# Kernel optimization log

Measured on AMD Instinct MI355X. Metric: run time of the kernel, lower is better.

Reference implementation:

```python
import jax, jax.numpy as jnp
import numpy as np

EPS = 1e-5

def _bn(x, g, b):
    # training-mode BatchNorm3d over (N, T, H, W) per channel (axis=1), biased variance
    red = (0, 2, 3, 4)
    m = x.mean(red, keepdims=True)
    v = x.var(red, keepdims=True)
    s = (1, -1, 1, 1, 1)
    return (x - m) / jnp.sqrt(v + EPS) * g.reshape(s) + b.reshape(s)

def _conv3d(x, w, b):
    # Conv3d kernel (1,3,3), padding (0,1,1)
    y = jax.lax.conv_general_dilated(x, w, (1, 1, 1), ((0, 0), (1, 1), (1, 1)),
                                     dimension_numbers=('NCDHW', 'OIDHW', 'NCDHW'))
    return y + b[None, :, None, None, None]

def _forward(x1, x2, attn_weight, W_up, b_up, W_mlp, b_mlp, g_mlp, be_mlp,
             W_c1, b_c1, g_c1, be_c1, W_c2, b_c2, g_c2, be_c2):
    w2 = W_up[:, :, 0]  # [Cin, Cout, 2, 2]
    y = jnp.einsum('bcthw,cokl->bothkwl', x1, w2)
    b_, o, t, h, k, w_, l = y.shape
    x1u = y.reshape(b_, o, t, h * k, w_ * l) + b_up[None, :, None, None, None]

    bs, d_in, T, H, W = x2.shape
    nH = attn_weight.shape[0]
    hh, ww = attn_weight.shape[2], attn_weight.shape[3]
    # [nH, bs, h, w, T, T] -> [nH*bs, T*T, h, w], bilinear upsample to (H, W)
    A = attn_weight.transpose(0, 1, 4, 5, 2, 3).reshape(nH * bs, T * T, hh, ww)
    A = jax.image.resize(A, (nH * bs, T * T, H, W), method='linear')
    A = A.reshape(nH, bs, T, T, H, W)
    # per-(head,b,H,W) temporal attention matmul: avoids materializing x2.repeat(n_head,...)
    ctx = jnp.einsum('nbtsxy,bcsxy->btxycn', A, x2)  # [bs,T,H,W,d_in,nH]
    ctx = ctx.reshape(bs, T, H, W, d_in * nH)        # flatten order (c, n) matches torch permute+view
    hmlp = jnp.einsum('btxyk,ko->btxyo', ctx, W_mlp) + b_mlp
    hmlp = hmlp.transpose(0, 4, 1, 2, 3)  # [bs, enc, T, H, W]
    hmlp = jax.nn.relu(_bn(hmlp, g_mlp, be_mlp))

    x = jnp.concatenate([hmlp, x1u], axis=1)  # [bs, enc+dec, T, H, W]
    x = jax.nn.relu(_bn(_conv3d(x, W_c1, b_c1), g_c1, be_c1))
    x = jax.nn.relu(_bn(_conv3d(x, W_c2, b_c2), g_c2, be_c2))
    return x

def setup_inputs() -> dict:
    key = jax.random.key(0)
    ks = jax.random.split(key, 8)
    bs, T, H, W = 2, 8, 128, 128
    dec, enc, nH = 64, 32, 4
    hh = ww = 16  # attn_scale_factor = 8
    return {
        'x1': jax.random.normal(ks[0], (bs, dec, T, H // 2, W // 2), jnp.float32),
        'x2': jax.random.normal(ks[1], (bs, enc, T, H, W), jnp.float32),
        'attn_weight': jax.random.uniform(ks[2], (nH, bs, hh, ww, T, T), jnp.float32),
        'W_up': jax.random.normal(ks[3], (dec, dec, 1, 2, 2), jnp.float32) * 0.05,
        'b_up': jnp.zeros((dec,), jnp.float32),
        'W_mlp': jax.random.normal(ks[4], (nH * enc, enc), jnp.float32) * 0.05,
        'b_mlp': jnp.zeros((enc,), jnp.float32),
        'g_mlp': jnp.ones((enc,), jnp.float32),
        'be_mlp': jnp.zeros((enc,), jnp.float32),
        'W_c1': jax.random.normal(ks[5], (enc, dec + enc, 1, 3, 3), jnp.float32) * 0.05,
        'b_c1': jnp.zeros((enc,), jnp.float32),
        'g_c1': jnp.ones((enc,), jnp.float32),
        'be_c1': jnp.zeros((enc,), jnp.float32),
        'W_c2': jax.random.normal(ks[6], (enc, enc, 1, 3, 3), jnp.float32) * 0.05,
        'b_c2': jnp.zeros((enc,), jnp.float32),
        'g_c2': jnp.ones((enc,), jnp.float32),
        'be_c2': jnp.zeros((enc,), jnp.float32),
    }

def reference(x1, x2, attn_weight, W_up, b_up, W_mlp, b_mlp, g_mlp, be_mlp,
              W_c1, b_c1, g_c1, be_c1, W_c2, b_c2, g_c2, be_c2):
    return _forward(x1, x2, attn_weight, W_up, b_up, W_mlp, b_mlp, g_mlp, be_mlp,
                    W_c1, b_c1, g_c1, be_c1, W_c2, b_c2, g_c2, be_c2)
```

## Files before the change

kernel.cpp:

```cpp
#include <hip/hip_runtime.h>


#define EPSV 1e-5f

typedef __attribute__((ext_vector_type(8))) short short8;
typedef __attribute__((ext_vector_type(4))) float floatx4;

__device__ inline short f2bf(float f) {
  union { float f; unsigned u; } v; v.f = f;
  unsigned r = (v.u + 0x7fffu + ((v.u >> 16) & 1u)) >> 16;
  return (short)r;
}
__device__ inline float bf2f(short s) {
  union { unsigned u; float f; } v; v.u = ((unsigned)(unsigned short)s) << 16;
  return v.f;
}

#define U_OFF    0
#define HMB_OFF  16777216
#define C1B_OFF  20971520
#define WB1_OFF  25165824
#define WB2_OFF  25179648
#define ST_OFF   25184256
#define SC_OFF   25184448

__global__ __launch_bounds__(256) void k_up(const float* __restrict__ x1,
        const float* __restrict__ Wup, const float* __restrict__ bup,
        float* __restrict__ U) {
  int bid = blockIdx.x;
  int hw = (bid & 15) * 256 + threadIdx.x;
  int t = (bid >> 4) & 7;
  int o = (bid >> 7) & 63;
  int b = bid >> 13;
  int h = hw >> 6, w = hw & 63;
  const float4* W4 = (const float4*)Wup;
  const float* xp = x1 + (b*64*8 + t)*4096 + hw;
  float a00=0.f, a01=0.f, a10=0.f, a11=0.f;
  #pragma unroll 8
  for (int c=0;c<64;++c) {
    float xv = xp[c*32768];
    float4 wv = W4[c*64+o];
    a00 = fmaf(xv, wv.x, a00);
    a01 = fmaf(xv, wv.y, a01);
    a10 = fmaf(xv, wv.z, a10);
    a11 = fmaf(xv, wv.w, a11);
  }
  float bb = bup[o];
  float* up = U + ((b*64+o)*8+t)*16384 + h*256 + w*2;
  ((float2*)up)[0]       = make_float2(a00+bb, a01+bb);
  ((float2*)(up+128))[0] = make_float2(a10+bb, a11+bb);
}

__global__ __launch_bounds__(256) void k_ctxmlp(const float* __restrict__ x2,
        const float* __restrict__ attn, const float* __restrict__ Wmlp,
        const float* __restrict__ bmlp, short* __restrict__ HMb) {
  int t = blockIdx.y, b = blockIdx.z;
  int pos = blockIdx.x*256 + threadIdx.x;
  __shared__ float la[8192];
  float4* la4 = (float4*)la;
  const float4* g4 = (const float4*)attn;
  #pragma unroll
  for (int k=0;k<8;++k) {
    int i = k*256 + (int)threadIdx.x;
    int s4 = i & 1, iy = (i>>1)&15, ix = (i>>5)&15, n = i>>9;
    la4[i] = g4[((((n*2+b)*16+ix)*16+iy)*8+t)*2 + s4];
  }
  __syncthreads();
  int x = pos >> 7, y = pos & 127;
  float ux = (x+0.5f)*0.125f - 0.5f;
  float uy = (y+0.5f)*0.125f - 0.5f;
  int ix0 = (int)floorf(ux), iy0 = (int)floorf(uy);
  float fx = ux - (float)ix0, fy = uy - (float)iy0;
  int ixa = max(ix0,0), ixb = min(ix0+1,15);
  int iya = max(iy0,0), iyb = min(iy0+1,15);
  float w00=(1.f-fx)*(1.f-fy), w01=(1.f-fx)*fy, w10=fx*(1.f-fy), w11=fx*fy;
  float a[4][8];
  #pragma unroll
  for (int n=0;n<4;++n) {
    const float4* p00 = la4 + ((n*16+ixa)*16+iya)*2;
    const float4* p01 = la4 + ((n*16+ixa)*16+iyb)*2;
    const float4* p10 = la4 + ((n*16+ixb)*16+iya)*2;
    const float4* p11 = la4 + ((n*16+ixb)*16+iyb)*2;
    #pragma unroll
    for (int q=0;q<2;++q) {
      float4 c00=p00[q], c01=p01[q], c10=p10[q], c11=p11[q];
      a[n][q*4+0] = w00*c00.x + w01*c01.x + w10*c10.x + w11*c11.x;
      a[n][q*4+1] = w00*c00.y + w01*c01.y + w10*c10.y + w11*c11.y;
      a[n][q*4+2] = w00*c00.z + w01*c01.z + w10*c10.z + w11*c11.z;
      a[n][q*4+3] = w00*c00.w + w01*c01.w + w10*c10.w + w11*c11.w;
    }
  }
  float acc[32];
  #pragma unroll
  for (int o=0;o<32;++o) acc[o] = bmlp[o];
  const float* x2p = x2 + b*4194304 + pos;
  #pragma unroll 4
  for (int c=0;c<32;++c) {
    float xr[8];
    #pragma unroll
    for (int s=0;s<8;++s) xr[s] = x2p[(c*8+s)*16384];
    #pragma unroll
    for (int n=0;n<4;++n) {
      float ctx = 0.f;
      #pragma unroll
      for (int s=0;s<8;++s) ctx = fmaf(a[n][s], xr[s], ctx);
      const float* wrow = Wmlp + (c*4+n)*32;
      #pragma unroll
      for (int o=0;o<32;++o) acc[o] = fmaf(ctx, wrow[o], acc[o]);
    }
  }
  short8* hp = (short8*)(HMb + ((long)((b*8+t)*16384 + pos)) * 32);
  #pragma unroll
  for (int g=0; g<4; ++g) {
    short8 v;
    #pragma unroll
    for (int j=0;j<8;++j) v[j] = f2bf(acc[g*8+j]);
    hp[g] = v;
  }
}

__global__ __launch_bounds__(256) void k_stats_cl(const unsigned* __restrict__ src, float* __restrict__ st) {
  __shared__ float sb[64];
  if (threadIdx.x < 64) sb[threadIdx.x] = 0.f;
  __syncthreads();
  int cp = threadIdx.x & 15;
  int pg = threadIdx.x >> 4;
  long pbase = (long)blockIdx.x * 256;
  float s0=0.f,q0=0.f,s1=0.f,q1=0.f;
  #pragma unroll 4
  for (int it = 0; it < 16; ++it) {
    long pos = pbase + it*16 + pg;
    unsigned d = src[pos*16 + cp];
    float v0 = bf2f((short)(d & 0xffffu));
    float v1 = bf2f((short)(d >> 16));
    s0+=v0; q0+=v0*v0; s1+=v1; q1+=v1*v1;
  }
  s0 += __shfl_xor(s0,16); s0 += __shfl_xor(s0,32);
  q0 += __shfl_xor(q0,16); q0 += __shfl_xor(q0,32);
  s1 += __shfl_xor(s1,16); s1 += __shfl_xor(s1,32);
  q1 += __shfl_xor(q1,16); q1 += __shfl_xor(q1,32);
  if ((threadIdx.x & 63) < 16) {
    atomicAdd(&sb[2*cp],    s0); atomicAdd(&sb[2*cp+1],    s1);
    atomicAdd(&sb[32+2*cp], q0); atomicAdd(&sb[32+2*cp+1], q1);
  }
  __syncthreads();
  if (threadIdx.x < 64) atomicAdd(&st[threadIdx.x], sb[threadIdx.x]);
}

__global__ __launch_bounds__(256) void k_stats(const float* __restrict__ src, float* __restrict__ st) {
  int bid = blockIdx.x;
  int span = bid & 31, ch = (bid>>5)&31, b = bid>>10;
  const float4* p4 = (const float4*)(src + (b*32+ch)*131072 + span*4096);
  float s=0.f, q=0.f;
  #pragma unroll
  for (int k=0;k<4;++k) {
    float4 v = p4[k*256 + threadIdx.x];
    s += v.x+v.y+v.z+v.w;
    q += v.x*v.x + v.y*v.y + v.z*v.z + v.w*v.w;
  }
  #pragma unroll
  for (int off=32; off>0; off>>=1) { s += __shfl_down(s,off); q += __shfl_down(q,off); }
  __shared__ float ls[4], lq[4];
  int lane = threadIdx.x & 63, wv = threadIdx.x >> 6;
  if (lane==0) { ls[wv]=s; lq[wv]=q; }
  __syncthreads();
  if (threadIdx.x==0) {
    atomicAdd(&st[ch],    ls[0]+ls[1]+ls[2]+ls[3]);
    atomicAdd(&st[32+ch], lq[0]+lq[1]+lq[2]+lq[3]);
  }
}

__global__ void k_finalize(const float* __restrict__ st, const float* __restrict__ g,
                           const float* __restrict__ be, float* __restrict__ sc, float* __restrict__ sh) {
  int c = threadIdx.x;
  if (c < 32) {
    float mean = st[c] * (1.f/262144.f);
    float var  = st[32+c] * (1.f/262144.f) - mean*mean;
    float s = g[c] / sqrtf(var + EPSV);
    sc[c] = s;
    sh[c] = be[c] - mean*s;
  }
}

__global__ __launch_bounds__(256) void k_repackb(const float* __restrict__ Wc1, const float* __restrict__ Wc2,
        short* __restrict__ wb1, short* __restrict__ wb2) {
  int i = blockIdx.x*256 + threadIdx.x;
  if (i < 27648) {
    int cc = i / 9216, r = i % 9216;
    int tap = r / 1024, r2 = r % 1024;
    int nt = r2 >> 9, lane = (r2 >> 3) & 63, j = r2 & 7;
    int o = nt*16 + (lane & 15);
    int cin = cc*32 + (lane >> 4)*8 + j;
    wb1[i] = f2bf(Wc1[(o*96 + cin)*9 + tap]);
  }
  if (i < 9216) {
    int tap = i / 1024, r2 = i % 1024;
    int nt = r2 >> 9, lane = (r2 >> 3) & 63, j = r2 & 7;
    int o = nt*16 + (lane & 15);
    int cin = (lane >> 4)*8 + j;
    wb2[i] = f2bf(Wc2[(o*32 + cin)*9 + tap]);
  }
}

template<int NCHUNK, bool FIRST>
__global__ __launch_bounds__(256) void k_conv_mfma(
    const short* __restrict__ srcCL, const float* __restrict__ srcU,
    const short* __restrict__ wb, const float* __restrict__ bias,
    const float* __restrict__ sc, const float* __restrict__ sh,
    short* __restrict__ dstCL, float* __restrict__ dstP) {
  constexpr int SMEM = FIRST ? 25920 : 33792;
  __shared__ __align__(16) char smem[SMEM];
  short* stage = (short*)smem;

  int t = blockIdx.y, b = blockIdx.z;
  int x0 = (int)(blockIdx.x >> 3) * 16, y0 = (int)(blockIdx.x & 7) * 16;
  int tid = threadIdx.x, lane = tid & 63, w = tid >> 6;

  float bias0 = bias[lane & 15], bias1 = bias[16 + (lane & 15)];
  floatx4 acc[4][2];
  #pragma unroll
  for (int mt=0; mt<4; ++mt) {
    acc[mt][0] = (floatx4){bias0,bias0,bias0,bias0};
    acc[mt][1] = (floatx4){bias1,bias1,bias1,bias1};
  }

  for (int cc=0; cc<NCHUNK; ++cc) {
    __syncthreads();
    if (cc == 0) {
      #pragma unroll
      for (int g=0; g<4; ++g) {
        float s0=sc[g*8+0],s1=sc[g*8+1],s2=sc[g*8+2],s3=sc[g*8+3];
        float s4=sc[g*8+4],s5=sc[g*8+5],s6=sc[g*8+6],s7=sc[g*8+7];
        float h0=sh[g*8+0],h1=sh[g*8+1],h2=sh[g*8+2],h3=sh[g*8+3];
        float h4=sh[g*8+4],h5=sh[g*8+5],h6=sh[g*8+6],h7=sh[g*8+7];
        for (int p=tid; p<324; p+=256) {
          int r = p/18, c = p - r*18;
          int X = x0 - 1 + r, Y = y0 - 1 + c;
          short8 val = (short8)0;
          if ((unsigned)X < 128u && (unsigned)Y < 128u) {
            short8 raw = *(const short8*)(srcCL + (((long)(b*8+t)*16384 + X*128 + Y) * 32 + g*8));
            val[0]=f2bf(fmaxf(fmaf(bf2f(raw[0]),s0,h0),0.f));
            val[1]=f2bf(fmaxf(fmaf(bf2f(raw[1]),s1,h1),0.f));
            val[2]=f2bf(fmaxf(fmaf(bf2f(raw[2]),s2,h2),0.f));
            val[3]=f2bf(fmaxf(fmaf(bf2f(raw[3]),s3,h3),0.f));
            val[4]=f2bf(fmaxf(fmaf(bf2f(raw[4]),s4,h4),0.f));
            val[5]=f2bf(fmaxf(fmaf(bf2f(raw[5]),s5,h5),0.f));
            val[6]=f2bf(fmaxf(fmaf(bf2f(raw[6]),s6,h6),0.f));
            val[7]=f2bf(fmaxf(fmaf(bf2f(raw[7]),s7,h7),0.f));
          }
          *(short8*)(stage + p*40 + g*8) = val;
        }
      }
    } else {
      int cbase = (cc-1)*32;
      #pragma unroll
      for (int g=0; g<4; ++g) {
        for (int p=tid; p<324; p+=256) {
          int r = p/18, c = p - r*18;
          int X = x0 - 1 + r, Y = y0 - 1 + c;
          short8 val = (short8)0;
          if ((unsigned)X < 128u && (unsigned)Y < 128u) {
            const float* up = srcU + ((long)(b*64 + cbase + g*8)*8 + t)*16384 + X*128 + Y;
            #pragma unroll
            for (int j=0;j<8;++j) val[j] = f2bf(up[(long)j*131072]);
          }
          *(short8*)(stage + p*40 + g*8) = val;
        }
      }
    }
    __syncthreads();
    const short8* wbp = (const short8*)wb + (long)cc*9*2*64;
    #pragma unroll
    for (int tap=0; tap<9; ++tap) {
      int dy = tap/3, dx = tap - dy*3;
      short8 b0 = wbp[(tap*2+0)*64 + lane];
      short8 b1 = wbp[(tap*2+1)*64 + lane];
      #pragma unroll
      for (int mt=0; mt<4; ++mt) {
        int p = (w*4 + mt + dy)*18 + (lane & 15) + dx;
        short8 a = *(const short8*)(stage + p*40 + (lane>>4)*8);
        acc[mt][0] = __builtin_amdgcn_mfma_f32_16x16x32_bf16(a, b0, acc[mt][0], 0,0,0);
        acc[mt][1] = __builtin_amdgcn_mfma_f32_16x16x32_bf16(a, b1, acc[mt][1], 0,0,0);
      }
    }
  }

  __syncthreads();
  if (FIRST) {
    short* tr = (short*)smem;
    #pragma unroll
    for (int mt=0; mt<4; ++mt) {
      int prow = w*4 + mt;
      #pragma unroll
      for (int nt=0; nt<2; ++nt) {
        #pragma unroll
        for (int r=0; r<4; ++r) {
          int m = (lane>>4)*4 + r;
          tr[(prow*16 + m)*32 + nt*16 + (lane&15)] = f2bf(acc[mt][nt][r]);
        }
      }
    }
    __syncthreads();
    int px = tid >> 4, py = tid & 15;
    short8* d8 = (short8*)(dstCL + (((long)(b*8+t)*128 + x0+px)*128 + (y0+py))*32);
    const short8* s8 = (const short8*)(tr + tid*32);
    d8[0]=s8[0]; d8[1]=s8[1]; d8[2]=s8[2]; d8[3]=s8[3];
  } else {
    float* trf = (float*)smem;
    #pragma unroll
    for (int mt=0; mt<4; ++mt) {
      int prow = w*4 + mt;
      #pragma unroll
      for (int nt=0; nt<2; ++nt) {
        #pragma unroll
        for (int r=0; r<4; ++r) {
          int m = (lane>>4)*4 + r;
          trf[(prow*16 + m)*33 + nt*16 + (lane&15)] = acc[mt][nt][r];
        }
      }
    }
    __syncthreads();
    int px = tid >> 4, py = tid & 15;
    #pragma unroll
    for (int ch=0; ch<32; ++ch) {
      dstP[((long)(b*32+ch)*8 + t)*16384 + (x0+px)*128 + (y0+py)] = trf[tid*33 + ch];
    }
  }
}

__global__ __launch_bounds__(256) void k_bnrelu(float* __restrict__ out,
        const float* __restrict__ sc, const float* __restrict__ sh) {
  int i = blockIdx.x*256 + threadIdx.x;
  int ch = (i >> 15) & 31;
  float s = sc[ch], h = sh[ch];
  float4* p = (float4*)out;
  float4 v = p[i];
  v.x = fmaxf(fmaf(v.x,s,h),0.f);
  v.y = fmaxf(fmaf(v.y,s,h),0.f);
  v.z = fmaxf(fmaf(v.z,s,h),0.f);
  v.w = fmaxf(fmaf(v.w,s,h),0.f);
  p[i] = v;
}

extern "C" void kernel_launch(void* const* d_in, const int* in_sizes, int n_in,
                              void* d_out, int out_size, void* d_ws, size_t ws_size,
                              hipStream_t stream) {
  (void)in_sizes; (void)n_in; (void)out_size; (void)ws_size;
  const float* x1   = (const float*)d_in[0];
  const float* x2   = (const float*)d_in[1];
  const float* attn = (const float*)d_in[2];
  const float* Wup  = (const float*)d_in[3];
  const float* bup  = (const float*)d_in[4];
  const float* Wmlp = (const float*)d_in[5];
  const float* bmlp = (const float*)d_in[6];
  const float* gmlp = (const float*)d_in[7];
  const float* bemlp= (const float*)d_in[8];
  const float* Wc1  = (const float*)d_in[9];
  const float* bc1  = (const float*)d_in[10];
  const float* gc1  = (const float*)d_in[11];
  const float* bec1 = (const float*)d_in[12];
  const float* Wc2  = (const float*)d_in[13];
  const float* bc2  = (const float*)d_in[14];
  const float* gc2  = (const float*)d_in[15];
  const float* bec2 = (const float*)d_in[16];
  float* ws  = (float*)d_ws;
  float* out = (float*)d_out;

  float* U    = ws + U_OFF;
  short* HMb  = (short*)(ws + HMB_OFF);
  short* C1b  = (short*)(ws + C1B_OFF);
  short* wb1  = (short*)(ws + WB1_OFF);
  short* wb2  = (short*)(ws + WB2_OFF);
  float* st1  = ws + ST_OFF;
  float* st2  = st1 + 64;
  float* st3  = st2 + 64;
  float* sc1  = ws + SC_OFF;  float* sh1 = sc1+32;
  float* sc2  = sh1+32;       float* sh2 = sc2+32;
  float* sc3  = sh2+32;       float* sh3 = sc3+32;

  hipMemsetAsync(st1, 0, 192*sizeof(float), stream);
  k_up<<<16384, 256, 0, stream>>>(x1, Wup, bup, U);
  k_repackb<<<108, 256, 0, stream>>>(Wc1, Wc2, wb1, wb2);
  k_ctxmlp<<<dim3(64,8,2), 256, 0, stream>>>(x2, attn, Wmlp, bmlp, HMb);
  k_stats_cl<<<1024, 256, 0, stream>>>((const unsigned*)HMb, st1);
  k_finalize<<<1, 32, 0, stream>>>(st1, gmlp, bemlp, sc1, sh1);
  k_conv_mfma<3,true><<<dim3(64,8,2), 256, 0, stream>>>(HMb, U, wb1, bc1, sc1, sh1, C1b, nullptr);
  k_stats_cl<<<1024, 256, 0, stream>>>((const unsigned*)C1b, st2);
  k_finalize<<<1, 32, 0, stream>>>(st2, gc1, bec1, sc2, sh2);
  k_conv_mfma<1,false><<<dim3(64,8,2), 256, 0, stream>>>(C1b, nullptr, wb2, bc2, sc2, sh2, nullptr, out);
  k_stats<<<2048, 256, 0, stream>>>(out, st3);
  k_finalize<<<1, 32, 0, stream>>>(st3, gc2, bec2, sc3, sh3);
  k_bnrelu<<<8192, 256, 0, stream>>>(out, sc3, sh3);
}
```

Before: 366.1 us.

## Use MFMA bf16 upsample, fuse BN stats into convs, bf16 channels-last intermediates

Replaces the scalar fp32 transposed-conv upsample with an MFMA bf16 kernel that writes a channels-last bf16 buffer, so conv1 can load the upsampled channels with vector loads. Both convolutions now accumulate the BatchNorm sum and sum-of-squares from their accumulators via shuffles and shared-memory atomics. This removes the separate stats passes. Conv2 writes bf16 channels-last output, and a new transposing BN+ReLU kernel produces the fp32 NCDHW result. The cost is extra bf16 rounding of the upsample and conv2 outputs, and BN statistics taken from fp32 accumulators before bf16 rounding.

```diff
diff --git a/kernel.cpp b/kernel.cpp
--- a/kernel.cpp
+++ b/kernel.cpp
@@ -4,6 +4,7 @@
 #define EPSV 1e-5f
 
 typedef __attribute__((ext_vector_type(8))) short short8;
+typedef __attribute__((ext_vector_type(4))) short short4v;
 typedef __attribute__((ext_vector_type(4))) float floatx4;
 
 __device__ inline short f2bf(float f) {
@@ -16,39 +17,106 @@
   return v.f;
 }
 
-#define U_OFF    0
-#define HMB_OFF  16777216
-#define C1B_OFF  20971520
-#define WB1_OFF  25165824
-#define WB2_OFF  25179648
-#define ST_OFF   25184256
-#define SC_OFF   25184448
-
-__global__ __launch_bounds__(256) void k_up(const float* __restrict__ x1,
-        const float* __restrict__ Wup, const float* __restrict__ bup,
-        float* __restrict__ U) {
-  int bid = blockIdx.x;
-  int hw = (bid & 15) * 256 + threadIdx.x;
-  int t = (bid >> 4) & 7;
-  int o = (bid >> 7) & 63;
-  int b = bid >> 13;
-  int h = hw >> 6, w = hw & 63;
-  const float4* W4 = (const float4*)Wup;
-  const float* xp = x1 + (b*64*8 + t)*4096 + hw;
-  float a00=0.f, a01=0.f, a10=0.f, a11=0.f;
-  #pragma unroll 8
-  for (int c=0;c<64;++c) {
-    float xv = xp[c*32768];
-    float4 wv = W4[c*64+o];
-    a00 = fmaf(xv, wv.x, a00);
-    a01 = fmaf(xv, wv.y, a01);
-    a10 = fmaf(xv, wv.z, a10);
-    a11 = fmaf(xv, wv.w, a11);
-  }
-  float bb = bup[o];
-  float* up = U + ((b*64+o)*8+t)*16384 + h*256 + w*2;
-  ((float2*)up)[0]       = make_float2(a00+bb, a01+bb);
-  ((float2*)(up+128))[0] = make_float2(a10+bb, a11+bb);
+#define UB_OFF   0
+#define HMB_OFF  8388608
+#define C1B_OFF  12582912
+#define C2B_OFF  16777216
+#define WB1_OFF  20971520
+#define WB2_OFF  20985344
+#define WUP_OFF  20989952
+#define ST_OFF   20998144
+#define SC_OFF   20998336
+
+__global__ __launch_bounds__(256) void k_repackb(const float* __restrict__ Wc1, const float* __restrict__ Wc2,
+        const float* __restrict__ Wup,
+        short* __restrict__ wb1, short* __restrict__ wb2, short* __restrict__ wupb) {
+  int i = blockIdx.x*256 + threadIdx.x;
+  if (i < 27648) {
+    int cc = i / 9216, r = i % 9216;
+    int tap = r / 1024, r2 = r % 1024;
+    int nt = r2 >> 9, lane = (r2 >> 3) & 63, j = r2 & 7;
+    int o = nt*16 + (lane & 15);
+    int cin = cc*32 + (lane >> 4)*8 + j;
+    wb1[i] = f2bf(Wc1[(o*96 + cin)*9 + tap]);
+  }
+  if (i < 9216) {
+    int tap = i / 1024, r2 = i % 1024;
+    int nt = r2 >> 9, lane = (r2 >> 3) & 63, j = r2 & 7;
+    int o = nt*16 + (lane & 15);
+    int cin = (lane >> 4)*8 + j;
+    wb2[i] = f2bf(Wc2[(o*32 + cin)*9 + tap]);
+  }
+  if (i < 16384) {
+    int j = i & 7, lane = (i >> 3) & 63, r = i >> 9;
+    int nt = r & 3, kb = (r >> 2) & 1, p = r >> 3;
+    int c = kb*32 + (lane >> 4)*8 + j;
+    int o = nt*16 + (lane & 15);
+    wupb[i] = f2bf(Wup[(c*64 + o)*4 + p]);
+  }
+}
+
+__global__ __launch_bounds__(256) void k_up_mfma(const float* __restrict__ x1,
+        const short* __restrict__ wupb, const float* __restrict__ bup,
+        short* __restrict__ Ub) {
+  __shared__ __align__(16) char smem[34816];
+  short8* stage = (short8*)smem;
+  int t = blockIdx.y, b = blockIdx.z;
+  int chunk = blockIdx.x >> 2, parity = blockIdx.x & 3;
+  int tid = threadIdx.x, lane = tid & 63, w = tid >> 6;
+
+  {
+    const float* xp = x1 + ((long)(b*64)*8 + t)*4096 + chunk*256 + tid;
+    #pragma unroll
+    for (int o8 = 0; o8 < 8; ++o8) {
+      short8 v;
+      #pragma unroll
+      for (int j = 0; j < 8; ++j) v[j] = f2bf(xp[(long)(o8*8+j)*32768]);
+      int kb = o8 >> 2, cq = o8 & 3;
+      stage[(kb*16 + (tid>>4))*64 + cq*16 + (tid&15)] = v;
+    }
+  }
+  __syncthreads();
+
+  floatx4 acc[4][4];
+  #pragma unroll
+  for (int nt=0; nt<4; ++nt) {
+    float bb = bup[nt*16 + (lane&15)];
+    #pragma unroll
+    for (int mt=0; mt<4; ++mt) acc[mt][nt] = (floatx4){bb,bb,bb,bb};
+  }
+  const short8* wp = (const short8*)wupb;
+  #pragma unroll
+  for (int kb=0; kb<2; ++kb) {
+    short8 bfr[4];
+    #pragma unroll
+    for (int nt=0; nt<4; ++nt) bfr[nt] = wp[((parity*2+kb)*4+nt)*64 + lane];
+    #pragma unroll
+    for (int mt=0; mt<4; ++mt) {
+      short8 a = stage[(kb*16 + w*4 + mt)*64 + lane];
+      #pragma unroll
+      for (int nt=0; nt<4; ++nt)
+        acc[mt][nt] = __builtin_amdgcn_mfma_f32_16x16x32_bf16(a, bfr[nt], acc[mt][nt], 0,0,0);
+    }
+  }
+
+  __syncthreads();
+  short* trb = (short*)smem;
+  #pragma unroll
+  for (int mt=0; mt<4; ++mt)
+    #pragma unroll
+    for (int nt=0; nt<4; ++nt)
+      #pragma unroll
+      for (int r=0; r<4; ++r)
+        trb[(w*64 + mt*16 + (lane>>4)*4 + r)*68 + nt*16 + (lane&15)] = f2bf(acc[mt][nt][r]);
+  __syncthreads();
+
+  int ip = chunk*256 + tid;
+  int X = 2*(ip>>6) + (parity>>1), Y = 2*(ip&63) + (parity&1);
+  short* dst = Ub + (((long)(b*8+t)*16384 + X*128 + Y)*64);
+  const short* src = trb + tid*68;
+  #pragma unroll
+  for (int k=0; k<16; ++k)
+    *(short4v*)(dst + k*4) = *(const short4v*)(src + k*4);
 }
 
 __global__ __launch_bounds__(256) void k_ctxmlp(const float* __restrict__ x2,
@@ -147,29 +215,6 @@
   if (threadIdx.x < 64) atomicAdd(&st[threadIdx.x], sb[threadIdx.x]);
 }
 
-__global__ __launch_bounds__(256) void k_stats(const float* __restrict__ src, float* __restrict__ st) {
-  int bid = blockIdx.x;
-  int span = bid & 31, ch = (bid>>5)&31, b = bid>>10;
-  const float4* p4 = (const float4*)(src + (b*32+ch)*131072 + span*4096);
-  float s=0.f, q=0.f;
-  #pragma unroll
-  for (int k=0;k<4;++k) {
-    float4 v = p4[k*256 + threadIdx.x];
-    s += v.x+v.y+v.z+v.w;
-    q += v.x*v.x + v.y*v.y + v.z*v.z + v.w*v.w;
-  }
-  #pragma unroll
-  for (int off=32; off>0; off>>=1) { s += __shfl_down(s,off); q += __shfl_down(q,off); }
-  __shared__ float ls[4], lq[4];
-  int lane = threadIdx.x & 63, wv = threadIdx.x >> 6;
-  if (lane==0) { ls[wv]=s; lq[wv]=q; }
-  __syncthreads();
-  if (threadIdx.x==0) {
-    atomicAdd(&st[ch],    ls[0]+ls[1]+ls[2]+ls[3]);
-    atomicAdd(&st[32+ch], lq[0]+lq[1]+lq[2]+lq[3]);
-  }
-}
-
 __global__ void k_finalize(const float* __restrict__ st, const float* __restrict__ g,
                            const float* __restrict__ be, float* __restrict__ sc, float* __restrict__ sh) {
   int c = threadIdx.x;
@@ -182,39 +227,20 @@
   }
 }
 
-__global__ __launch_bounds__(256) void k_repackb(const float* __restrict__ Wc1, const float* __restrict__ Wc2,
-        short* __restrict__ wb1, short* __restrict__ wb2) {
-  int i = blockIdx.x*256 + threadIdx.x;
-  if (i < 27648) {
-    int cc = i / 9216, r = i % 9216;
-    int tap = r / 1024, r2 = r % 1024;
-    int nt = r2 >> 9, lane = (r2 >> 3) & 63, j = r2 & 7;
-    int o = nt*16 + (lane & 15);
-    int cin = cc*32 + (lane >> 4)*8 + j;
-    wb1[i] = f2bf(Wc1[(o*96 + cin)*9 + tap]);
-  }
-  if (i < 9216) {
-    int tap = i / 1024, r2 = i % 1024;
-    int nt = r2 >> 9, lane = (r2 >> 3) & 63, j = r2 & 7;
-    int o = nt*16 + (lane & 15);
-    int cin = (lane >> 4)*8 + j;
-    wb2[i] = f2bf(Wc2[(o*32 + cin)*9 + tap]);
-  }
-}
-
-template<int NCHUNK, bool FIRST>
+template<int NCHUNK>
 __global__ __launch_bounds__(256) void k_conv_mfma(
-    const short* __restrict__ srcCL, const float* __restrict__ srcU,
+    const short* __restrict__ srcCL, const short* __restrict__ srcU,
     const short* __restrict__ wb, const float* __restrict__ bias,
     const float* __restrict__ sc, const float* __restrict__ sh,
-    short* __restrict__ dstCL, float* __restrict__ dstP) {
-  constexpr int SMEM = FIRST ? 25920 : 33792;
-  __shared__ __align__(16) char smem[SMEM];
+    short* __restrict__ dstCL, float* __restrict__ st) {
+  __shared__ __align__(16) char smem[25920];
+  __shared__ float sbuf[64];
   short* stage = (short*)smem;
 
   int t = blockIdx.y, b = blockIdx.z;
   int x0 = (int)(blockIdx.x >> 3) * 16, y0 = (int)(blockIdx.x & 7) * 16;
   int tid = threadIdx.x, lane = tid & 63, w = tid >> 6;
+  if (tid < 64) sbuf[tid] = 0.f;
 
   float bias0 = bias[lane & 15], bias1 = bias[16 + (lane & 15)];
   floatx4 acc[4][2];
@@ -223,6 +249,7 @@
     acc[mt][0] = (floatx4){bias0,bias0,bias0,bias0};
     acc[mt][1] = (floatx4){bias1,bias1,bias1,bias1};
   }
+  long slab = (long)(b*8+t)*16384;
 
   for (int cc=0; cc<NCHUNK; ++cc) {
     __syncthreads();
@@ -238,7 +265,7 @@
           int X = x0 - 1 + r, Y = y0 - 1 + c;
           short8 val = (short8)0;
           if ((unsigned)X < 128u && (unsigned)Y < 128u) {
-            short8 raw = *(const short8*)(srcCL + (((long)(b*8+t)*16384 + X*128 + Y) * 32 + g*8));
+            short8 raw = *(const short8*)(srcCL + ((slab + X*128 + Y) * 32 + g*8));
             val[0]=f2bf(fmaxf(fmaf(bf2f(raw[0]),s0,h0),0.f));
             val[1]=f2bf(fmaxf(fmaf(bf2f(raw[1]),s1,h1),0.f));
             val[2]=f2bf(fmaxf(fmaf(bf2f(raw[2]),s2,h2),0.f));
@@ -260,9 +287,7 @@
           int X = x0 - 1 + r, Y = y0 - 1 + c;
           short8 val = (short8)0;
           if ((unsigned)X < 128u && (unsigned)Y < 128u) {
-            const float* up = srcU + ((long)(b*64 + cbase + g*8)*8 + t)*16384 + X*128 + Y;
-            #pragma unroll
-            for (int j=0;j<8;++j) val[j] = f2bf(up[(long)j*131072]);
+            val = *(const short8*)(srcU + ((slab + X*128 + Y) * 64 + cbase + g*8));
           }
           *(short8*)(stage + p*40 + g*8) = val;
         }
@@ -285,61 +310,76 @@
     }
   }
 
-  __syncthreads();
-  if (FIRST) {
-    short* tr = (short*)smem;
-    #pragma unroll
-    for (int mt=0; mt<4; ++mt) {
-      int prow = w*4 + mt;
-      #pragma unroll
-      for (int nt=0; nt<2; ++nt) {
-        #pragma unroll
-        for (int r=0; r<4; ++r) {
-          int m = (lane>>4)*4 + r;
-          tr[(prow*16 + m)*32 + nt*16 + (lane&15)] = f2bf(acc[mt][nt][r]);
-        }
+  float s0=0.f,q0=0.f,s1=0.f,q1=0.f;
+  #pragma unroll
+  for (int mt=0; mt<4; ++mt)
+    #pragma unroll
+    for (int r=0; r<4; ++r) {
+      float v0 = acc[mt][0][r]; s0 += v0; q0 += v0*v0;
+      float v1 = acc[mt][1][r]; s1 += v1; q1 += v1*v1;
+    }
+  s0 += __shfl_xor(s0,16); s0 += __shfl_xor(s0,32);
+  q0 += __shfl_xor(q0,16); q0 += __shfl_xor(q0,32);
+  s1 += __shfl_xor(s1,16); s1 += __shfl_xor(s1,32);
+  q1 += __shfl_xor(q1,16); q1 += __shfl_xor(q1,32);
+
+  __syncthreads();
+  if (lane < 16) {
+    atomicAdd(&sbuf[lane],    s0); atomicAdd(&sbuf[16+lane], s1);
+    atomicAdd(&sbuf[32+lane], q0); atomicAdd(&sbuf[48+lane], q1);
+  }
+  short* tr = (short*)smem;
+  #pragma unroll
+  for (int mt=0; mt<4; ++mt) {
+    int prow = w*4 + mt;
+    #pragma unroll
+    for (int nt=0; nt<2; ++nt) {
+      #pragma unroll
+      for (int r=0; r<4; ++r) {
+        int m = (lane>>4)*4 + r;
+        tr[(prow*16 + m)*32 + nt*16 + (lane&15)] = f2bf(acc[mt][nt][r]);
       }
     }
-    __syncthreads();
-    int px = tid >> 4, py = tid & 15;
-    short8* d8 = (short8*)(dstCL + (((long)(b*8+t)*128 + x0+px)*128 + (y0+py))*32);
-    const short8* s8 = (const short8*)(tr + tid*32);
-    d8[0]=s8[0]; d8[1]=s8[1]; d8[2]=s8[2]; d8[3]=s8[3];
-  } else {
-    float* trf = (float*)smem;
-    #pragma unroll
-    for (int mt=0; mt<4; ++mt) {
-      int prow = w*4 + mt;
-      #pragma unroll
-      for (int nt=0; nt<2; ++nt) {
-        #pragma unroll
-        for (int r=0; r<4; ++r) {
-          int m = (lane>>4)*4 + r;
-          trf[(prow*16 + m)*33 + nt*16 + (lane&15)] = acc[mt][nt][r];
-        }
+  }
+  __syncthreads();
+  int px = tid >> 4, py = tid & 15;
+  short8* d8 = (short8*)(dstCL + ((slab + (long)(x0+px)*128 + (y0+py))*32));
+  const short8* s8 = (const short8*)(tr + tid*32);
+  d8[0]=s8[0]; d8[1]=s8[1]; d8[2]=s8[2]; d8[3]=s8[3];
+  if (tid < 64) atomicAdd(&st[tid], sbuf[tid]);
+}
+
+__global__ __launch_bounds__(256) void k_bnrelu2(const short* __restrict__ C2b,
+        const float* __restrict__ sc, const float* __restrict__ sh,
+        float* __restrict__ out) {
+  __shared__ float tb[10592];
+  int t = blockIdx.y, b = blockIdx.z;
+  int posbase = blockIdx.x * 256;
+  int tid = threadIdx.x;
+  long slab = (long)(b*8+t)*16384;
+  {
+    const short8* sp = (const short8*)(C2b + (slab + posbase + tid)*32);
+    int pi = tid + (tid>>5)*8;
+    #pragma unroll
+    for (int g=0; g<4; ++g) {
+      short8 v = sp[g];
+      #pragma unroll
+      for (int j=0; j<8; ++j) {
+        int ch = g*8+j;
+        tb[ch*321 + pi] = fmaxf(fmaf(bf2f(v[j]), sc[ch], sh[ch]), 0.f);
       }
     }
-    __syncthreads();
-    int px = tid >> 4, py = tid & 15;
-    #pragma unroll
-    for (int ch=0; ch<32; ++ch) {
-      dstP[((long)(b*32+ch)*8 + t)*16384 + (x0+px)*128 + (y0+py)] = trf[tid*33 + ch];
-    }
-  }
-}
-
-__global__ __launch_bounds__(256) void k_bnrelu(float* __restrict__ out,
-        const float* __restrict__ sc, const float* __restrict__ sh) {
-  int i = blockIdx.x*256 + threadIdx.x;
-  int ch = (i >> 15) & 31;
-  float s = sc[ch], h = sh[ch];
-  float4* p = (float4*)out;
-  float4 v = p[i];
-  v.x = fmaxf(fmaf(v.x,s,h),0.f);
-  v.y = fmaxf(fmaf(v.y,s,h),0.f);
-  v.z = fmaxf(fmaf(v.z,s,h),0.f);
-  v.w = fmaxf(fmaf(v.w,s,h),0.f);
-  p[i] = v;
+  }
+  __syncthreads();
+  int ch = tid >> 3, pg = tid & 7;
+  float* op = out + ((long)(b*32+ch)*8 + t)*16384 + posbase + pg*32;
+  const float* tp = tb + ch*321 + pg*40;
+  #pragma unroll
+  for (int k=0; k<8; ++k) {
+    float4 v;
+    v.x = tp[k*4+0]; v.y = tp[k*4+1]; v.z = tp[k*4+2]; v.w = tp[k*4+3];
+    *(float4*)(op + k*4) = v;
+  }
 }
 
 extern "C" void kernel_launch(void* const* d_in, const int* in_sizes, int n_in,
@@ -366,11 +406,13 @@
   float* ws  = (float*)d_ws;
   float* out = (float*)d_out;
 
-  float* U    = ws + U_OFF;
+  short* Ub   = (short*)(ws + UB_OFF);
   short* HMb  = (short*)(ws + HMB_OFF);
   short* C1b  = (short*)(ws + C1B_OFF);
+  short* C2b  = (short*)(ws + C2B_OFF);
   short* wb1  = (short*)(ws + WB1_OFF);
   short* wb2  = (short*)(ws + WB2_OFF);
+  short* wupb = (short*)(ws + WUP_OFF);
   float* st1  = ws + ST_OFF;
   float* st2  = st1 + 64;
   float* st3  = st2 + 64;
@@ -379,16 +421,14 @@
   float* sc3  = sh2+32;       float* sh3 = sc3+32;
 
   hipMemsetAsync(st1, 0, 192*sizeof(float), stream);
-  k_up<<<16384, 256, 0, stream>>>(x1, Wup, bup, U);
-  k_repackb<<<108, 256, 0, stream>>>(Wc1, Wc2, wb1, wb2);
+  k_repackb<<<108, 256, 0, stream>>>(Wc1, Wc2, Wup, wb1, wb2, wupb);
+  k_up_mfma<<<dim3(64,8,2), 256, 0, stream>>>(x1, wupb, bup, Ub);
   k_ctxmlp<<<dim3(64,8,2), 256, 0, stream>>>(x2, attn, Wmlp, bmlp, HMb);
   k_stats_cl<<<1024, 256, 0, stream>>>((const unsigned*)HMb, st1);
   k_finalize<<<1, 32, 0, stream>>>(st1, gmlp, bemlp, sc1, sh1);
-  k_conv_mfma<3,true><<<dim3(64,8,2), 256, 0, stream>>>(HMb, U, wb1, bc1, sc1, sh1, C1b, nullptr);
-  k_stats_cl<<<1024, 256, 0, stream>>>((const unsigned*)C1b, st2);
+  k_conv_mfma<3><<<dim3(64,8,2), 256, 0, stream>>>(HMb, Ub, wb1, bc1, sc1, sh1, C1b, st2);
   k_finalize<<<1, 32, 0, stream>>>(st2, gc1, bec1, sc2, sh2);
-  k_conv_mfma<1,false><<<dim3(64,8,2), 256, 0, stream>>>(C1b, nullptr, wb2, bc2, sc2, sh2, nullptr, out);
-  k_stats<<<2048, 256, 0, stream>>>(out, st3);
+  k_conv_mfma<1><<<dim3(64,8,2), 256, 0, stream>>>(C1b, nullptr, wb2, bc2, sc2, sh2, C2b, st3);
   k_finalize<<<1, 32, 0, stream>>>(st3, gc2, bec2, sc3, sh3);
-  k_bnrelu<<<8192, 256, 0, stream>>>(out, sc3, sh3);
-}
+  k_bnrelu2<<<dim3(64,8,2), 256, 0, stream>>>(C2b, sc3, sh3, out);
+}
```

Result: faster. 322.9 us (-11.8%).
